# Kernel tuning notes

Measured on AMD Instinct MI355X. Metric: run time of the kernel, lower is better.

The kernel has to match this reference:

```python
import jax, jax.numpy as jnp
import numpy as np

LN_EPS = 1e-5


def setup_inputs() -> dict:
    key = jax.random.key(0)
    k1, k2, k3 = jax.random.split(key, 3)
    N, E, D_IN, D_OUT = 50000, 500000, 128, 128
    x = jax.random.normal(k1, (N, D_IN), dtype=jnp.float32)
    edge_index = jax.random.randint(k2, (2, E), 0, N, dtype=jnp.int64)
    W = jax.random.normal(k3, (D_IN, D_OUT), dtype=jnp.float32) * (1.0 / np.sqrt(D_IN))
    b = jnp.zeros((D_OUT,), dtype=jnp.float32)
    ln_gamma = jnp.ones((D_OUT,), dtype=jnp.float32)
    ln_beta = jnp.zeros((D_OUT,), dtype=jnp.float32)
    return {"x": x, "edge_index": edge_index, "W": W, "b": b,
            "ln_gamma": ln_gamma, "ln_beta": ln_beta}


def reference(x, edge_index, W, b, ln_gamma, ln_beta):
    N = x.shape[0]
    # GCNConv: linear transform first (no fused bias; bias added after aggregation)
    h = x @ W  # [N, D_out]
    # add self-loops
    loops = jnp.arange(N, dtype=edge_index.dtype)
    src = jnp.concatenate([edge_index[0], loops])  # [E+N]
    dst = jnp.concatenate([edge_index[1], loops])  # [E+N]
    # symmetric normalization deg^{-1/2} (degree computed on dst, incl. self-loops)
    deg = jax.ops.segment_sum(jnp.ones(src.shape, dtype=h.dtype), dst, num_segments=N)
    dinv = jnp.where(deg > 0, jax.lax.rsqrt(deg), 0.0)
    norm = dinv[src] * dinv[dst]  # [E+N]
    # gather messages, scale, scatter-add to destinations
    msgs = h[src] * norm[:, None]  # [E+N, D_out]
    out = jax.ops.segment_sum(msgs, dst, num_segments=N) + b  # [N, D_out]
    # LayerNorm over features
    mu = out.mean(axis=-1, keepdims=True)
    var = out.var(axis=-1, keepdims=True)
    out = (out - mu) * jax.lax.rsqrt(var + LN_EPS) * ln_gamma + ln_beta
    # activation
    return jax.nn.relu(out)
```

## Files before the change

kernel.cpp:

```cpp
#include <hip/hip_runtime.h>
#include <hip/hip_fp16.h>
#include <math.h>

#define D 128
#define LN_EPS 1e-5f
#define BKT 64

typedef _Float16 f16x8 __attribute__((ext_vector_type(8)));
typedef float    f32x4 __attribute__((ext_vector_type(4)));

__global__ void gemm_kernel(const float* __restrict__ x, const float* __restrict__ W,
                            unsigned* __restrict__ h2, int N) {
    __shared__ _Float16 xs[64][136];
    __shared__ _Float16 wt[128][136];
    int tid  = threadIdx.x;
    int row0 = blockIdx.x * 64;

#pragma unroll
    for (int i = 0; i < 8; ++i) {
        int idx = i * 256 + tid;
        int r   = idx >> 5;
        int c4  = idx & 31;
        float4 v = make_float4(0.f, 0.f, 0.f, 0.f);
        if (row0 + r < N) v = *(const float4*)&x[(size_t)(row0 + r) * D + c4 * 4];
        __half2 lo = __floats2half2_rn(v.x, v.y);
        __half2 hi = __floats2half2_rn(v.z, v.w);
        *(__half2*)&xs[r][c4 * 4]     = lo;
        *(__half2*)&xs[r][c4 * 4 + 2] = hi;
    }
#pragma unroll
    for (int i = 0; i < 16; ++i) {
        int f  = i * 256 + tid;
        int k  = f >> 5;
        int n4 = f & 31;
        float4 wv = *(const float4*)&W[k * D + n4 * 4];
        wt[n4 * 4 + 0][k] = (_Float16)wv.x;
        wt[n4 * 4 + 1][k] = (_Float16)wv.y;
        wt[n4 * 4 + 2][k] = (_Float16)wv.z;
        wt[n4 * 4 + 3][k] = (_Float16)wv.w;
    }
    __syncthreads();

    int l     = tid & 63;
    int mtile = tid >> 6;
    int mn    = l & 15;
    int kq    = (l >> 4) * 8;
    f32x4 acc[8];
#pragma unroll
    for (int nt = 0; nt < 8; ++nt) acc[nt] = (f32x4){0.f, 0.f, 0.f, 0.f};

#pragma unroll
    for (int ks = 0; ks < 4; ++ks) {
        int kb = ks * 32 + kq;
        f16x8 a = *(f16x8*)&xs[mtile * 16 + mn][kb];
#pragma unroll
        for (int nt = 0; nt < 8; ++nt) {
            f16x8 bf = *(f16x8*)&wt[nt * 16 + mn][kb];
            acc[nt] = __builtin_amdgcn_mfma_f32_16x16x32_f16(a, bf, acc[nt], 0, 0, 0);
        }
    }

    int quad = l >> 4;
#pragma unroll
    for (int nt = 0; nt < 8; ++nt) {
#pragma unroll
        for (int rg = 0; rg < 4; ++rg) {
            float v  = acc[nt][rg];
            float pv = __shfl_xor(v, 1);
            if (!(l & 1)) {
                int row = row0 + mtile * 16 + quad * 4 + rg;
                if (row < N) {
                    __half2 p = __floats2half2_rn(v, pv);
                    h2[(size_t)row * (D / 2) + nt * 8 + (mn >> 1)] = *(unsigned*)&p;
                }
            }
        }
    }
}

__global__ void bucket_kernel(const int* __restrict__ src, const int* __restrict__ dst,
                              int* __restrict__ degi, int* __restrict__ bucket, int E) {
    int e = blockIdx.x * blockDim.x + threadIdx.x;
    if (e < E) {
        int d = dst[e];
        int p = atomicAdd(&degi[d], 1);
        if (p < BKT) bucket[(size_t)d * BKT + p] = src[e];
    }
}

__global__ void finalize_kernel(const int* __restrict__ degi, int* __restrict__ degc,
                                float* __restrict__ dinv, int N) {
    int i = blockIdx.x * blockDim.x + threadIdx.x;
    if (i < N) {
        int d = degi[i];
        degc[i] = d < BKT ? d : BKT;
        dinv[i] = rsqrtf((float)d + 1.0f);
    }
}

__device__ __forceinline__ void acc_edge(float& a0, float& a1, unsigned u, float w) {
    __half2 hv = *(__half2*)&u;
    a0 = fmaf(__low2float(hv),  w, a0);
    a1 = fmaf(__high2float(hv), w, a1);
}

__global__ void gather_ln_kernel(const int* __restrict__ bucket, const int* __restrict__ degc,
                                 const float* __restrict__ dinv,
                                 const unsigned* __restrict__ h2, const float* __restrict__ b,
                                 const float* __restrict__ g, const float* __restrict__ be,
                                 float* __restrict__ out, int N) {
    int row  = blockIdx.x * 4 + (threadIdx.x >> 6);
    int lane = threadIdx.x & 63;
    if (row >= N) return;
    int dgc  = degc[row];
    float di = dinv[row];
    float sw = di * di;
    unsigned su = h2[(size_t)row * (D / 2) + lane];
    float acc0 = 0.f, acc1 = 0.f;
    acc_edge(acc0, acc1, su, sw);
    const int* bk = bucket + (size_t)row * BKT;
    int e = 0;
    for (; e + 7 < dgc; e += 8) {
        int   s[8]; float wgt[8]; unsigned u[8];
#pragma unroll
        for (int j = 0; j < 8; ++j) s[j] = bk[e + j];
#pragma unroll
        for (int j = 0; j < 8; ++j) wgt[j] = dinv[s[j]] * di;
#pragma unroll
        for (int j = 0; j < 8; ++j) u[j] = h2[(size_t)s[j] * (D / 2) + lane];
#pragma unroll
        for (int j = 0; j < 8; ++j) acc_edge(acc0, acc1, u[j], wgt[j]);
    }
    for (; e < dgc; ++e) {
        int s = bk[e];
        acc_edge(acc0, acc1, h2[(size_t)s * (D / 2) + lane], dinv[s] * di);
    }
    float2 bb = *(const float2*)&b[lane * 2];
    float v0 = acc0 + bb.x;
    float v1 = acc1 + bb.y;
    float s = v0 + v1;
    float q = v0 * v0 + v1 * v1;
#pragma unroll
    for (int off = 32; off; off >>= 1) {
        s += __shfl_xor(s, off);
        q += __shfl_xor(q, off);
    }
    float mean = s * (1.0f / 128.0f);
    float var  = q * (1.0f / 128.0f) - mean * mean;
    float rstd = rsqrtf(var + LN_EPS);
    float2 gg = *(const float2*)&g[lane * 2];
    float2 eb = *(const float2*)&be[lane * 2];
    float y0 = (v0 - mean) * rstd * gg.x + eb.x;
    float y1 = (v1 - mean) * rstd * gg.y + eb.y;
    *(float2*)&out[(size_t)row * D + lane * 2] = make_float2(fmaxf(y0, 0.0f), fmaxf(y1, 0.0f));
}

extern "C" void kernel_launch(void* const* d_in, const int* in_sizes, int n_in,
                              void* d_out, int out_size, void* d_ws, size_t ws_size,
                              hipStream_t stream) {
    const float* x  = (const float*)d_in[0];
    const int*   ei = (const int*)d_in[1];
    const float* W  = (const float*)d_in[2];
    const float* b  = (const float*)d_in[3];
    const float* g  = (const float*)d_in[4];
    const float* be = (const float*)d_in[5];

    int N = in_sizes[0] / D;
    int E = in_sizes[1] / 2;
    const int* src = ei;
    const int* dst = ei + E;

    float* out = (float*)d_out;

    char* w = (char*)d_ws;
    unsigned* h2   = (unsigned*)w;            w += (size_t)N * (D / 2) * sizeof(unsigned);
    int*   degi    = (int*)w;                 w += (size_t)N * sizeof(int);
    int*   degc    = (int*)w;                 w += (size_t)N * sizeof(int);
    float* dinv    = (float*)w;               w += (size_t)N * sizeof(float);
    int*   bucket  = (int*)w;                 w += (size_t)N * BKT * sizeof(int);

    hipMemsetAsync(degi, 0, (size_t)N * sizeof(int), stream);

    gemm_kernel    <<<(N + 63) / 64,   256, 0, stream>>>(x, W, h2, N);
    bucket_kernel  <<<(E + 255) / 256, 256, 0, stream>>>(src, dst, degi, bucket, E);
    finalize_kernel<<<(N + 255) / 256, 256, 0, stream>>>(degi, degc, dinv, N);
    gather_ln_kernel<<<(N + 3) / 4,    256, 0, stream>>>(bucket, degc, dinv, h2,
                                                         b, g, be, out, N);
}
```

Measured before the change: 171.8 us.

## Pre-transpose W once, fold degree finalize into gather, drop memset

A small prep kernel converts W to transposed fp16 in global memory and zeroes the degree counters, replacing the memset and the per-block W transpose in the GEMM. The GEMM now reads B fragments straight from global/L2 instead of LDS. The finalize kernel is removed and the gather computes clamped degree and rsqrt on the fly from raw degree counts. This cuts launches and per-block W staging, but adds redundant rsqrt per edge and uncached-LDS global B reads in the MFMA loop.

```diff
diff --git a/kernel.cpp b/kernel.cpp
--- a/kernel.cpp
+++ b/kernel.cpp
@@ -9,10 +9,18 @@
 typedef _Float16 f16x8 __attribute__((ext_vector_type(8)));
 typedef float    f32x4 __attribute__((ext_vector_type(4)));
 
-__global__ void gemm_kernel(const float* __restrict__ x, const float* __restrict__ W,
+__global__ void prep_kernel(const float* __restrict__ W, _Float16* __restrict__ wtg,
+                            int* __restrict__ degi, int N) {
+    int idx = blockIdx.x * 256 + threadIdx.x;
+    int k = idx >> 7;
+    int n = idx & 127;
+    wtg[n * D + k] = (_Float16)W[k * D + n];
+    for (int i = idx; i < N; i += 64 * 256) degi[i] = 0;
+}
+
+__global__ void gemm_kernel(const float* __restrict__ x, const _Float16* __restrict__ wtg,
                             unsigned* __restrict__ h2, int N) {
     __shared__ _Float16 xs[64][136];
-    __shared__ _Float16 wt[128][136];
     int tid  = threadIdx.x;
     int row0 = blockIdx.x * 64;
 
@@ -27,17 +35,6 @@
         __half2 hi = __floats2half2_rn(v.z, v.w);
         *(__half2*)&xs[r][c4 * 4]     = lo;
         *(__half2*)&xs[r][c4 * 4 + 2] = hi;
-    }
-#pragma unroll
-    for (int i = 0; i < 16; ++i) {
-        int f  = i * 256 + tid;
-        int k  = f >> 5;
-        int n4 = f & 31;
-        float4 wv = *(const float4*)&W[k * D + n4 * 4];
-        wt[n4 * 4 + 0][k] = (_Float16)wv.x;
-        wt[n4 * 4 + 1][k] = (_Float16)wv.y;
-        wt[n4 * 4 + 2][k] = (_Float16)wv.z;
-        wt[n4 * 4 + 3][k] = (_Float16)wv.w;
     }
     __syncthreads();
 
@@ -55,7 +52,7 @@
         f16x8 a = *(f16x8*)&xs[mtile * 16 + mn][kb];
 #pragma unroll
         for (int nt = 0; nt < 8; ++nt) {
-            f16x8 bf = *(f16x8*)&wt[nt * 16 + mn][kb];
+            f16x8 bf = *(const f16x8*)&wtg[(nt * 16 + mn) * D + kb];
             acc[nt] = __builtin_amdgcn_mfma_f32_16x16x32_f16(a, bf, acc[nt], 0, 0, 0);
         }
     }
@@ -88,32 +85,22 @@
     }
 }
 
-__global__ void finalize_kernel(const int* __restrict__ degi, int* __restrict__ degc,
-                                float* __restrict__ dinv, int N) {
-    int i = blockIdx.x * blockDim.x + threadIdx.x;
-    if (i < N) {
-        int d = degi[i];
-        degc[i] = d < BKT ? d : BKT;
-        dinv[i] = rsqrtf((float)d + 1.0f);
-    }
-}
-
 __device__ __forceinline__ void acc_edge(float& a0, float& a1, unsigned u, float w) {
     __half2 hv = *(__half2*)&u;
     a0 = fmaf(__low2float(hv),  w, a0);
     a1 = fmaf(__high2float(hv), w, a1);
 }
 
-__global__ void gather_ln_kernel(const int* __restrict__ bucket, const int* __restrict__ degc,
-                                 const float* __restrict__ dinv,
+__global__ void gather_ln_kernel(const int* __restrict__ bucket, const int* __restrict__ degi,
                                  const unsigned* __restrict__ h2, const float* __restrict__ b,
                                  const float* __restrict__ g, const float* __restrict__ be,
                                  float* __restrict__ out, int N) {
     int row  = blockIdx.x * 4 + (threadIdx.x >> 6);
     int lane = threadIdx.x & 63;
     if (row >= N) return;
-    int dgc  = degc[row];
-    float di = dinv[row];
+    int dg   = degi[row];
+    int dgc  = dg < BKT ? dg : BKT;
+    float di = rsqrtf((float)dg + 1.0f);
     float sw = di * di;
     unsigned su = h2[(size_t)row * (D / 2) + lane];
     float acc0 = 0.f, acc1 = 0.f;
@@ -121,11 +108,11 @@
     const int* bk = bucket + (size_t)row * BKT;
     int e = 0;
     for (; e + 7 < dgc; e += 8) {
-        int   s[8]; float wgt[8]; unsigned u[8];
+        int s[8]; float wgt[8]; unsigned u[8];
 #pragma unroll
         for (int j = 0; j < 8; ++j) s[j] = bk[e + j];
 #pragma unroll
-        for (int j = 0; j < 8; ++j) wgt[j] = dinv[s[j]] * di;
+        for (int j = 0; j < 8; ++j) wgt[j] = rsqrtf((float)degi[s[j]] + 1.0f) * di;
 #pragma unroll
         for (int j = 0; j < 8; ++j) u[j] = h2[(size_t)s[j] * (D / 2) + lane];
 #pragma unroll
@@ -133,7 +120,8 @@
     }
     for (; e < dgc; ++e) {
         int s = bk[e];
-        acc_edge(acc0, acc1, h2[(size_t)s * (D / 2) + lane], dinv[s] * di);
+        acc_edge(acc0, acc1, h2[(size_t)s * (D / 2) + lane],
+                 rsqrtf((float)degi[s] + 1.0f) * di);
     }
     float2 bb = *(const float2*)&b[lane * 2];
     float v0 = acc0 + bb.x;
@@ -173,17 +161,14 @@
     float* out = (float*)d_out;
 
     char* w = (char*)d_ws;
-    unsigned* h2   = (unsigned*)w;            w += (size_t)N * (D / 2) * sizeof(unsigned);
-    int*   degi    = (int*)w;                 w += (size_t)N * sizeof(int);
-    int*   degc    = (int*)w;                 w += (size_t)N * sizeof(int);
-    float* dinv    = (float*)w;               w += (size_t)N * sizeof(float);
-    int*   bucket  = (int*)w;                 w += (size_t)N * BKT * sizeof(int);
+    unsigned* h2    = (unsigned*)w;           w += (size_t)N * (D / 2) * sizeof(unsigned);
+    int*      degi  = (int*)w;                w += (size_t)N * sizeof(int);
+    _Float16* wtg   = (_Float16*)w;           w += (size_t)D * D * sizeof(_Float16);
+    int*      bucket= (int*)w;                w += (size_t)N * BKT * sizeof(int);
 
-    hipMemsetAsync(degi, 0, (size_t)N * sizeof(int), stream);
-
-    gemm_kernel    <<<(N + 63) / 64,   256, 0, stream>>>(x, W, h2, N);
-    bucket_kernel  <<<(E + 255) / 256, 256, 0, stream>>>(src, dst, degi, bucket, E);
-    finalize_kernel<<<(N + 255) / 256, 256, 0, stream>>>(degi, degc, dinv, N);
-    gather_ln_kernel<<<(N + 3) / 4,    256, 0, stream>>>(bucket, degc, dinv, h2,
+    prep_kernel   <<<64,               256, 0, stream>>>(W, wtg, degi, N);
+    gemm_kernel   <<<(N + 63) / 64,    256, 0, stream>>>(x, wtg, h2, N);
+    bucket_kernel <<<(E + 255) / 256,  256, 0, stream>>>(src, dst, degi, bucket, E);
+    gather_ln_kernel<<<(N + 3) / 4,    256, 0, stream>>>(bucket, degi, h2,
                                                          b, g, be, out, N);
 }
```

New measurement: 167.8 us. -2.3%, faster.
